# Kernel tuning notes

Measured on AMD Instinct MI355X. Metric: run time of the kernel, lower is better.

Reference implementation:

```python
import jax, jax.numpy as jnp
import numpy as np

THETA = 1.0       # spiking threshold (params['neuron']['theta'])
TAU_SR = 10.0     # SRM synaptic time constant (tauSr)
K = 100           # srm kernel support; alpha kernel has decayed to ~0 by 10*tau


def srm_kernel():
    # SLAYER SRMALPHA kernel: eps(t) = (t/tau) * exp(1 - t/tau), t = 0..K-1 (Ts = 1)
    t = jnp.arange(K, dtype=jnp.float32)
    return (t / TAU_SR) * jnp.exp(1.0 - t / TAU_SR)


def psp(x):
    # Causal temporal convolution with shared SRM kernel: y[t] = sum_s eps[s] * x[t-s]
    # x: [B, C, T]
    B, C, T = x.shape
    k = srm_kernel()[::-1].reshape(1, 1, K)  # flip: lax conv is correlation
    xr = x.reshape(B * C, 1, T)
    y = jax.lax.conv_general_dilated(xr, k, window_strides=(1,), padding=[(K - 1, 0)])
    return y.reshape(B, C, T)


def spike(u):
    # Hard threshold (forward of SLAYER spike function)
    return (u >= THETA).astype(u.dtype)


def setup_inputs() -> dict:
    key = jax.random.key(0)
    k1, k2, k3 = jax.random.split(key, 3)
    B, T = 256, 1000
    IN, HID, OUT = 78, 16, 20
    spike_input = (jax.random.uniform(k1, (B, IN, T)) < 0.1).astype(jnp.float32)
    W1 = jax.random.normal(k2, (HID, IN), dtype=jnp.float32) * 0.3
    W2 = jax.random.normal(k3, (OUT, HID), dtype=jnp.float32) * 0.3
    return {"spike_input": spike_input, "W1": W1, "W2": W2}


def reference(spike_input, W1, W2):
    # layer 1: dense (per-timestep matmul) -> psp temporal filter -> spike threshold
    u1 = psp(jnp.einsum('hi,bit->bht', W1, spike_input))  # [B, HID, T]
    s1 = spike(u1)
    # layer 2
    u2 = psp(jnp.einsum('oh,bht->bot', W2, s1))           # [B, OUT, T]
    return spike(u2)
```

## Files before the change

### kernel.cpp

```cpp
#include <hip/hip_runtime.h>
#include <math.h>


#define B_     256
#define IN_    78
#define HID_   16
#define OUT_   20
#define T_     1000
#define TT_    125
#define J_     224
#define ZSTR_  228
#define XSTR_  260

#define GRP(EP, A0,A1,A2,A3, B0,B1,B2,B3, C0,C1,C2) { \
  const double2 e01_ = *(const double2*)(EP); \
  const double2 e23_ = *(const double2*)((EP)+2); \
  u0 += e01_.x*(A3); u1 += e01_.x*(B0); u2 += e01_.x*(B1); u3 += e01_.x*(B2); \
  u4 += e01_.x*(B3); u5 += e01_.x*(C0); u6 += e01_.x*(C1); u7 += e01_.x*(C2); \
  u0 += e01_.y*(A2); u1 += e01_.y*(A3); u2 += e01_.y*(B0); u3 += e01_.y*(B1); \
  u4 += e01_.y*(B2); u5 += e01_.y*(B3); u6 += e01_.y*(C0); u7 += e01_.y*(C1); \
  u0 += e23_.x*(A1); u1 += e23_.x*(A2); u2 += e23_.x*(A3); u3 += e23_.x*(B0); \
  u4 += e23_.x*(B1); u5 += e23_.x*(B2); u6 += e23_.x*(B3); u7 += e23_.x*(C0); \
  u0 += e23_.y*(A0); u1 += e23_.y*(A1); u2 += e23_.y*(A2); u3 += e23_.y*(A3); \
  u4 += e23_.y*(B0); u5 += e23_.y*(B1); u6 += e23_.y*(B2); u7 += e23_.y*(B3); }

#define LOADF(X0,X1,X2,X3, P) { \
  const float4 lf_ = *(const float4*)(P); \
  X0 = (double)lf_.x; X1 = (double)lf_.y; X2 = (double)lf_.z; X3 = (double)lf_.w; }

__device__ __forceinline__ void init_eps_d(double* eps_d, int tid) {
  if (tid < 100) {
    float a = (float)tid / 10.0f;
    float e = a * expf(1.0f - a);
    eps_d[tid] = (double)e;
  }
}

#define MMROW(XR, W0, W1) { \
  const float2 f0_ = *(const float2*)((XR)); \
  const float2 f1_ = *(const float2*)((XR) + 64); \
  const float2 f2_ = *(const float2*)((XR) + 128); \
  const float2 f3_ = *(const float2*)((XR) + 192); \
  const double x0_=(double)f0_.x, x1_=(double)f0_.y; \
  const double x2_=(double)f1_.x, x3_=(double)f1_.y; \
  const double x4_=(double)f2_.x, x5_=(double)f2_.y; \
  const double x6_=(double)f3_.x, x7_=(double)f3_.y; \
  m00 += (W0)*x0_; m01 += (W0)*x1_; m02 += (W0)*x2_; m03 += (W0)*x3_; \
  m04 += (W0)*x4_; m05 += (W0)*x5_; m06 += (W0)*x6_; m07 += (W0)*x7_; \
  m10 += (W1)*x0_; m11 += (W1)*x1_; m12 += (W1)*x2_; m13 += (W1)*x3_; \
  m14 += (W1)*x4_; m15 += (W1)*x5_; m16 += (W1)*x6_; m17 += (W1)*x7_; }

#define STORE2(BASE, EOFF, MA, MB) \
  if (tb + (EOFF) < T_ - 1) \
    *(float2*)&zout[(BASE) + (size_t)(tb + (EOFF))] = \
        make_float2((float)(MA), (float)(MB));

__global__ __launch_bounds__(256) void mm1(
    const float* __restrict__ x, const float* __restrict__ W1,
    float* __restrict__ zout)
{
  __shared__ float  xs[13 * XSTR_];
  __shared__ double wd[16 * 80];

  const int tid = threadIdx.x;
  const int b   = blockIdx.x >> 2;
  const int tc  = blockIdx.x & 3;
  const int tcb = tc * 256;

  for (int idx = tid; idx < HID_ * IN_; idx += 256)
    wd[(idx / IN_) * 80 + (idx % IN_)] = (double)W1[idx];

  const int  t_c = tcb + tid;
  const bool cok = (t_c < T_);
  const int p = tid >> 5;
  const int q = tid & 31;

  double m00=0,m01=0,m02=0,m03=0,m04=0,m05=0,m06=0,m07=0;
  double m10=0,m11=0,m12=0,m13=0,m14=0,m15=0,m16=0,m17=0;

  for (int ci = 0; ci < 6; ++ci) {
    __syncthreads();
    {
      const float* xp = x + ((size_t)b * IN_ + ci * 13) * T_ + t_c;
#pragma unroll
      for (int r = 0; r < 13; ++r)
        xs[r * XSTR_ + tid] = cok ? xp[r * T_] : 0.0f;
    }
    __syncthreads();
    const int wbase0 = (2*p)     * 80 + ci * 13;
    const int wbase1 = (2*p + 1) * 80 + ci * 13;
#pragma unroll
    for (int i = 0; i < 13; ++i) {
      const float* xr = &xs[i * XSTR_ + 2 * q];
      const double w0 = wd[wbase0 + i];
      const double w1 = wd[wbase1 + i];
      MMROW(xr, w0, w1)
    }
  }

  const size_t r0 = ((size_t)b * HID_ + 2*p) * T_;
  const size_t r1 = r0 + T_;
  const int tb = tcb + 2 * q;
  STORE2(r0,   0, m00, m01)  STORE2(r0,  64, m02, m03)
  STORE2(r0, 128, m04, m05)  STORE2(r0, 192, m06, m07)
  STORE2(r1,   0, m10, m11)  STORE2(r1,  64, m12, m13)
  STORE2(r1, 128, m14, m15)  STORE2(r1, 192, m16, m17)
}

__global__ __launch_bounds__(256) void mm2(
    const float* __restrict__ s1, const float* __restrict__ W2,
    float* __restrict__ zout)
{
  __shared__ float  ss[16 * XSTR_];
  __shared__ double wd[OUT_ * HID_];

  const int tid = threadIdx.x;
  const int b   = blockIdx.x >> 2;
  const int tc  = blockIdx.x & 3;
  const int tcb = tc * 256;

  for (int idx = tid; idx < OUT_ * HID_; idx += 256)
    wd[idx] = (double)W2[idx];

  const int  t_c = tcb + tid;
  const bool cok = (t_c < T_);
  {
    const float* sp = s1 + (size_t)b * HID_ * T_ + t_c;
#pragma unroll
    for (int r = 0; r < HID_; ++r)
      ss[r * XSTR_ + tid] = cok ? sp[r * T_] : 0.0f;
  }
  __syncthreads();

  const int p = tid >> 5;
  const int q = tid & 31;
  const int tb = tcb + 2 * q;

  for (int pg = p; pg < 10; pg += 8) {
    double m00=0,m01=0,m02=0,m03=0,m04=0,m05=0,m06=0,m07=0;
    double m10=0,m11=0,m12=0,m13=0,m14=0,m15=0,m16=0,m17=0;
    const int wbase0 = (2*pg)     * HID_;
    const int wbase1 = (2*pg + 1) * HID_;
#pragma unroll
    for (int i = 0; i < HID_; ++i) {
      const float* xr = &ss[i * XSTR_ + 2 * q];
      const double w0 = wd[wbase0 + i];
      const double w1 = wd[wbase1 + i];
      MMROW(xr, w0, w1)
    }
    const size_t r0 = ((size_t)b * OUT_ + 2*pg) * T_;
    const size_t r1 = r0 + T_;
    STORE2(r0,   0, m00, m01)  STORE2(r0,  64, m02, m03)
    STORE2(r0, 128, m04, m05)  STORE2(r0, 192, m06, m07)
    STORE2(r1,   0, m10, m11)  STORE2(r1,  64, m12, m13)
    STORE2(r1, 128, m14, m15)  STORE2(r1, 192, m16, m17)
  }
}

__global__ __launch_bounds__(256) void fir_g(
    const float* __restrict__ zin, float* __restrict__ sout,
    int R, int tile_fixed)
{
  __shared__ float zf[OUT_ * ZSTR_];
  __shared__ __align__(16) double eps_d[100];

  const int tid  = threadIdx.x;
  const int b    = (tile_fixed >= 0) ? (int)blockIdx.x : (int)(blockIdx.x >> 3);
  const int tile = (tile_fixed >= 0) ? tile_fixed      : (int)(blockIdx.x & 7);
  const int t0   = tile * TT_;

  init_eps_d(eps_d, tid);
  for (int idx = tid; idx < R * ZSTR_; idx += 256) {
    const int cc = idx % ZSTR_;
    const int t  = t0 - 99 + cc;
    const int r  = idx / ZSTR_;
    zf[idx] = (cc < J_ && t >= 0) ? zin[((size_t)b * R + r) * T_ + t] : 0.0f;
  }
  __syncthreads();

  for (int task = tid; task < R * 16; task += 256) {
    const int h = task >> 4, q = task & 15;
    const float* zrow = &zf[h * ZSTR_ + 8 * q];
    double u0=0,u1=0,u2=0,u3=0,u4=0,u5=0,u6=0,u7=0;
    double A0,A1,A2,A3,B0,B1,B2,B3,C0,C1,C2,C3;
    LOADF(A0,A1,A2,A3, zrow + 96);
    LOADF(B0,B1,B2,B3, zrow + 100);
    LOADF(C0,C1,C2,C3, zrow + 104);
    GRP(eps_d, A0,A1,A2,A3, B0,B1,B2,B3, C0,C1,C2)

    const float*  zp = zrow + 92;
    const double* ep = eps_d + 4;
#pragma unroll 1
    for (int k = 0; k < 8; ++k) {
      LOADF(C0,C1,C2,C3, zp);
      GRP(ep,     C0,C1,C2,C3, A0,A1,A2,A3, B0,B1,B2)
      LOADF(B0,B1,B2,B3, zp - 4);
      GRP(ep + 4, B0,B1,B2,B3, C0,C1,C2,C3, A0,A1,A2)
      LOADF(A0,A1,A2,A3, zp - 8);
      GRP(ep + 8, A0,A1,A2,A3, B0,B1,B2,B3, C0,C1,C2)
      zp -= 12; ep += 12;
    }

    const size_t base = ((size_t)b * R + h) * T_ + t0 + 8 * q;
    const int tb = 8 * q;
    const float f0=(float)u0, f1=(float)u1, f2=(float)u2, f3=(float)u3;
    const float f4=(float)u4, f5=(float)u5, f6=(float)u6, f7=(float)u7;
    sout[base + 0] = (f0 >= 1.0f) ? 1.0f : 0.0f;
    sout[base + 1] = (f1 >= 1.0f) ? 1.0f : 0.0f;
    sout[base + 2] = (f2 >= 1.0f) ? 1.0f : 0.0f;
    sout[base + 3] = (f3 >= 1.0f) ? 1.0f : 0.0f;
    if (tb + 4 < TT_) sout[base + 4] = (f4 >= 1.0f) ? 1.0f : 0.0f;
    if (tb + 5 < TT_) sout[base + 5] = (f5 >= 1.0f) ? 1.0f : 0.0f;
    if (tb + 6 < TT_) sout[base + 6] = (f6 >= 1.0f) ? 1.0f : 0.0f;
    if (tb + 7 < TT_) sout[base + 7] = (f7 >= 1.0f) ? 1.0f : 0.0f;
  }
}

extern "C" void kernel_launch(void* const* d_in, const int* in_sizes, int n_in,
                              void* d_out, int out_size, void* d_ws, size_t ws_size,
                              hipStream_t stream) {
  const float* x  = (const float*)d_in[0];
  const float* W1 = (const float*)d_in[1];
  const float* W2 = (const float*)d_in[2];
  float* outp = (float*)d_out;
  float* base = (float*)d_ws;

  const size_t Z1E = (size_t)B_ * HID_ * T_;
  const size_t Z2E = (size_t)B_ * OUT_ * T_;

  if (ws_size >= (Z1E + Z2E) * sizeof(float)) {
    float* z1 = base;
    float* s1 = base + Z2E;
    float* z2 = base;
    mm1<<<dim3(B_ * 4), dim3(256), 0, stream>>>(x, W1, z1);
    fir_g<<<dim3(B_ * 8), dim3(256), 0, stream>>>(z1, s1, HID_, -1);
    mm2<<<dim3(B_ * 4), dim3(256), 0, stream>>>(s1, W2, z2);
    fir_g<<<dim3(B_ * 8), dim3(256), 0, stream>>>(z2, outp, OUT_, -1);
  } else if (ws_size >= 2 * Z1E * sizeof(float)) {
    float* z1 = base;
    float* s1 = base + Z1E;
    mm1<<<dim3(B_ * 4), dim3(256), 0, stream>>>(x, W1, z1);
    fir_g<<<dim3(B_ * 8), dim3(256), 0, stream>>>(z1, s1, HID_, -1);
    mm2<<<dim3(B_ * 4), dim3(256), 0, stream>>>(s1, W2, outp);
    for (int k = 7; k >= 0; --k)
      fir_g<<<dim3(B_), dim3(256), 0, stream>>>(outp, outp, OUT_, k);
  } else {
    float* z1 = base;
    mm1<<<dim3(B_ * 4), dim3(256), 0, stream>>>(x, W1, z1);
    for (int k = 7; k >= 0; --k)
      fir_g<<<dim3(B_), dim3(256), 0, stream>>>(z1, z1, HID_, k);
    mm2<<<dim3(B_ * 4), dim3(256), 0, stream>>>(z1, W2, outp);
    for (int k = 7; k >= 0; --k)
      fir_g<<<dim3(B_), dim3(256), 0, stream>>>(outp, outp, OUT_, k);
  }
}
```

Before: 122.6 us.

## Halve time tile in mm kernels and prefetch next input chunk into registers

The two channel-mixing kernels now cover 128 timesteps per block instead of 256, which doubles the grid and halves the per-thread accumulators from 16 to 8 doubles. The load pattern changes so that 256 threads cover 128 columns by two rows each. mm1 also software-pipelines its six input-channel chunks: the next chunk's global loads go into registers before the current chunk's FMAs run. The aim is more parallelism and latency hiding, at the cost of more blocks and more redundant weight staging into shared memory per block.

```diff
diff --git a/kernel.cpp b/kernel.cpp
--- a/kernel.cpp
+++ b/kernel.cpp
@@ -10,7 +10,8 @@
 #define TT_    125
 #define J_     224
 #define ZSTR_  228
-#define XSTR_  260
+#define TC_    128
+#define MSTR_  132
 
 #define GRP(EP, A0,A1,A2,A3, B0,B1,B2,B3, C0,C1,C2) { \
   const double2 e01_ = *(const double2*)(EP); \
@@ -36,19 +37,13 @@
   }
 }
 
-#define MMROW(XR, W0, W1) { \
-  const float2 f0_ = *(const float2*)((XR)); \
+#define MMROW2(XR, W0, W1) { \
+  const float2 f0_ = *(const float2*)(XR); \
   const float2 f1_ = *(const float2*)((XR) + 64); \
-  const float2 f2_ = *(const float2*)((XR) + 128); \
-  const float2 f3_ = *(const float2*)((XR) + 192); \
   const double x0_=(double)f0_.x, x1_=(double)f0_.y; \
   const double x2_=(double)f1_.x, x3_=(double)f1_.y; \
-  const double x4_=(double)f2_.x, x5_=(double)f2_.y; \
-  const double x6_=(double)f3_.x, x7_=(double)f3_.y; \
   m00 += (W0)*x0_; m01 += (W0)*x1_; m02 += (W0)*x2_; m03 += (W0)*x3_; \
-  m04 += (W0)*x4_; m05 += (W0)*x5_; m06 += (W0)*x6_; m07 += (W0)*x7_; \
-  m10 += (W1)*x0_; m11 += (W1)*x1_; m12 += (W1)*x2_; m13 += (W1)*x3_; \
-  m14 += (W1)*x4_; m15 += (W1)*x5_; m16 += (W1)*x6_; m17 += (W1)*x7_; }
+  m10 += (W1)*x0_; m11 += (W1)*x1_; m12 += (W1)*x2_; m13 += (W1)*x3_; }
 
 #define STORE2(BASE, EOFF, MA, MB) \
   if (tb + (EOFF) < T_ - 1) \
@@ -59,101 +54,112 @@
     const float* __restrict__ x, const float* __restrict__ W1,
     float* __restrict__ zout)
 {
-  __shared__ float  xs[13 * XSTR_];
+  __shared__ float  xs[13 * MSTR_];
   __shared__ double wd[16 * 80];
 
   const int tid = threadIdx.x;
-  const int b   = blockIdx.x >> 2;
-  const int tc  = blockIdx.x & 3;
-  const int tcb = tc * 256;
+  const int b   = blockIdx.x >> 3;
+  const int tc  = blockIdx.x & 7;
+  const int tcb = tc * TC_;
 
   for (int idx = tid; idx < HID_ * IN_; idx += 256)
     wd[(idx / IN_) * 80 + (idx % IN_)] = (double)W1[idx];
 
-  const int  t_c = tcb + tid;
-  const bool cok = (t_c < T_);
+  const int  c_  = tid & 127;
+  const int  r0_ = tid >> 7;
+  const int  tg_ = tcb + c_;
+  const bool tok = (tg_ < T_);
+  const bool t6  = tok && (r0_ == 0);
+
   const int p = tid >> 5;
   const int q = tid & 31;
 
-  double m00=0,m01=0,m02=0,m03=0,m04=0,m05=0,m06=0,m07=0;
-  double m10=0,m11=0,m12=0,m13=0,m14=0,m15=0,m16=0,m17=0;
-
+  double m00=0,m01=0,m02=0,m03=0,m10=0,m11=0,m12=0,m13=0;
+  float g0,g1,g2,g3,g4,g5,g6;
+
+#define ISSUE_MM1(CI) { \
+    const float* xb_ = x + ((size_t)b * IN_ + (CI) * 13 + r0_) * T_ + tg_; \
+    g0 = tok ? xb_[0]       : 0.0f; \
+    g1 = tok ? xb_[2  * T_] : 0.0f; \
+    g2 = tok ? xb_[4  * T_] : 0.0f; \
+    g3 = tok ? xb_[6  * T_] : 0.0f; \
+    g4 = tok ? xb_[8  * T_] : 0.0f; \
+    g5 = tok ? xb_[10 * T_] : 0.0f; \
+    g6 = t6  ? xb_[12 * T_] : 0.0f; }
+
+  ISSUE_MM1(0)
   for (int ci = 0; ci < 6; ++ci) {
     __syncthreads();
     {
-      const float* xp = x + ((size_t)b * IN_ + ci * 13) * T_ + t_c;
-#pragma unroll
-      for (int r = 0; r < 13; ++r)
-        xs[r * XSTR_ + tid] = cok ? xp[r * T_] : 0.0f;
+      float* dst = &xs[r0_ * MSTR_ + c_];
+      dst[0]          = g0;  dst[2  * MSTR_] = g1;
+      dst[4  * MSTR_] = g2;  dst[6  * MSTR_] = g3;
+      dst[8  * MSTR_] = g4;  dst[10 * MSTR_] = g5;
+      if (r0_ == 0) dst[12 * MSTR_] = g6;
     }
     __syncthreads();
+    if (ci < 5) ISSUE_MM1(ci + 1)
     const int wbase0 = (2*p)     * 80 + ci * 13;
     const int wbase1 = (2*p + 1) * 80 + ci * 13;
 #pragma unroll
     for (int i = 0; i < 13; ++i) {
-      const float* xr = &xs[i * XSTR_ + 2 * q];
-      const double w0 = wd[wbase0 + i];
-      const double w1 = wd[wbase1 + i];
-      MMROW(xr, w0, w1)
-    }
-  }
-
-  const size_t r0 = ((size_t)b * HID_ + 2*p) * T_;
-  const size_t r1 = r0 + T_;
+      const float* xr = &xs[i * MSTR_ + 2 * q];
+      MMROW2(xr, wd[wbase0 + i], wd[wbase1 + i])
+    }
+  }
+
+  const size_t r0s = ((size_t)b * HID_ + 2*p) * T_;
+  const size_t r1s = r0s + T_;
   const int tb = tcb + 2 * q;
-  STORE2(r0,   0, m00, m01)  STORE2(r0,  64, m02, m03)
-  STORE2(r0, 128, m04, m05)  STORE2(r0, 192, m06, m07)
-  STORE2(r1,   0, m10, m11)  STORE2(r1,  64, m12, m13)
-  STORE2(r1, 128, m14, m15)  STORE2(r1, 192, m16, m17)
+  STORE2(r0s,  0, m00, m01)  STORE2(r0s, 64, m02, m03)
+  STORE2(r1s,  0, m10, m11)  STORE2(r1s, 64, m12, m13)
 }
 
 __global__ __launch_bounds__(256) void mm2(
     const float* __restrict__ s1, const float* __restrict__ W2,
     float* __restrict__ zout)
 {
-  __shared__ float  ss[16 * XSTR_];
+  __shared__ float  ss[16 * MSTR_];
   __shared__ double wd[OUT_ * HID_];
 
   const int tid = threadIdx.x;
-  const int b   = blockIdx.x >> 2;
-  const int tc  = blockIdx.x & 3;
-  const int tcb = tc * 256;
+  const int b   = blockIdx.x >> 3;
+  const int tc  = blockIdx.x & 7;
+  const int tcb = tc * TC_;
 
   for (int idx = tid; idx < OUT_ * HID_; idx += 256)
     wd[idx] = (double)W2[idx];
 
-  const int  t_c = tcb + tid;
-  const bool cok = (t_c < T_);
   {
-    const float* sp = s1 + (size_t)b * HID_ * T_ + t_c;
+    const int  c_  = tid & 127;
+    const int  r0_ = tid >> 7;
+    const int  tg_ = tcb + c_;
+    const bool tok = (tg_ < T_);
+    const float* sb = s1 + ((size_t)b * HID_ + r0_) * T_ + tg_;
+    float* dst = &ss[r0_ * MSTR_ + c_];
 #pragma unroll
-    for (int r = 0; r < HID_; ++r)
-      ss[r * XSTR_ + tid] = cok ? sp[r * T_] : 0.0f;
+    for (int e = 0; e < 8; ++e)
+      dst[2 * e * MSTR_] = tok ? sb[2 * e * T_] : 0.0f;
   }
   __syncthreads();
 
-  const int p = tid >> 5;
-  const int q = tid & 31;
+  const int p  = tid >> 5;
+  const int q  = tid & 31;
   const int tb = tcb + 2 * q;
 
   for (int pg = p; pg < 10; pg += 8) {
-    double m00=0,m01=0,m02=0,m03=0,m04=0,m05=0,m06=0,m07=0;
-    double m10=0,m11=0,m12=0,m13=0,m14=0,m15=0,m16=0,m17=0;
+    double m00=0,m01=0,m02=0,m03=0,m10=0,m11=0,m12=0,m13=0;
     const int wbase0 = (2*pg)     * HID_;
     const int wbase1 = (2*pg + 1) * HID_;
 #pragma unroll
     for (int i = 0; i < HID_; ++i) {
-      const float* xr = &ss[i * XSTR_ + 2 * q];
-      const double w0 = wd[wbase0 + i];
-      const double w1 = wd[wbase1 + i];
-      MMROW(xr, w0, w1)
-    }
-    const size_t r0 = ((size_t)b * OUT_ + 2*pg) * T_;
-    const size_t r1 = r0 + T_;
-    STORE2(r0,   0, m00, m01)  STORE2(r0,  64, m02, m03)
-    STORE2(r0, 128, m04, m05)  STORE2(r0, 192, m06, m07)
-    STORE2(r1,   0, m10, m11)  STORE2(r1,  64, m12, m13)
-    STORE2(r1, 128, m14, m15)  STORE2(r1, 192, m16, m17)
+      const float* xr = &ss[i * MSTR_ + 2 * q];
+      MMROW2(xr, wd[wbase0 + i], wd[wbase1 + i])
+    }
+    const size_t r0s = ((size_t)b * OUT_ + 2*pg) * T_;
+    const size_t r1s = r0s + T_;
+    STORE2(r0s,  0, m00, m01)  STORE2(r0s, 64, m02, m03)
+    STORE2(r1s,  0, m10, m11)  STORE2(r1s, 64, m12, m13)
   }
 }
 
@@ -232,24 +238,24 @@
     float* z1 = base;
     float* s1 = base + Z2E;
     float* z2 = base;
-    mm1<<<dim3(B_ * 4), dim3(256), 0, stream>>>(x, W1, z1);
+    mm1<<<dim3(B_ * 8), dim3(256), 0, stream>>>(x, W1, z1);
     fir_g<<<dim3(B_ * 8), dim3(256), 0, stream>>>(z1, s1, HID_, -1);
-    mm2<<<dim3(B_ * 4), dim3(256), 0, stream>>>(s1, W2, z2);
+    mm2<<<dim3(B_ * 8), dim3(256), 0, stream>>>(s1, W2, z2);
     fir_g<<<dim3(B_ * 8), dim3(256), 0, stream>>>(z2, outp, OUT_, -1);
   } else if (ws_size >= 2 * Z1E * sizeof(float)) {
     float* z1 = base;
     float* s1 = base + Z1E;
-    mm1<<<dim3(B_ * 4), dim3(256), 0, stream>>>(x, W1, z1);
+    mm1<<<dim3(B_ * 8), dim3(256), 0, stream>>>(x, W1, z1);
     fir_g<<<dim3(B_ * 8), dim3(256), 0, stream>>>(z1, s1, HID_, -1);
-    mm2<<<dim3(B_ * 4), dim3(256), 0, stream>>>(s1, W2, outp);
+    mm2<<<dim3(B_ * 8), dim3(256), 0, stream>>>(s1, W2, outp);
     for (int k = 7; k >= 0; --k)
       fir_g<<<dim3(B_), dim3(256), 0, stream>>>(outp, outp, OUT_, k);
   } else {
     float* z1 = base;
-    mm1<<<dim3(B_ * 4), dim3(256), 0, stream>>>(x, W1, z1);
+    mm1<<<dim3(B_ * 8), dim3(256), 0, stream>>>(x, W1, z1);
     for (int k = 7; k >= 0; --k)
       fir_g<<<dim3(B_), dim3(256), 0, stream>>>(z1, z1, HID_, k);
-    mm2<<<dim3(B_ * 4), dim3(256), 0, stream>>>(z1, W2, outp);
+    mm2<<<dim3(B_ * 8), dim3(256), 0, stream>>>(z1, W2, outp);
     for (int k = 7; k >= 0; --k)
       fir_g<<<dim3(B_), dim3(256), 0, stream>>>(outp, outp, OUT_, k);
   }
```

After: 109.8 us. 1.12x faster.

## Fuse per-layer matmul with temporal FIR and spike into single kernels

Applied to the files above, without the earlier changes.

Merges each layer's dense matmul with its PSP convolution and threshold into one kernel per layer, tiled by batch and 125-step time windows with a 99-step halo. The pre-activation z stays in shared memory instead of making a round trip through global memory, and the launch count drops from four to two. In exchange, each tile recomputes the matmul over its halo region (224 columns computed for 125 outputs), and the larger shared-memory footprint per block may lower occupancy.

```diff
diff --git a/kernel.cpp b/kernel.cpp
--- a/kernel.cpp
+++ b/kernel.cpp
@@ -27,6 +27,25 @@
 #define LOADF(X0,X1,X2,X3, P) { \
   const float4 lf_ = *(const float4*)(P); \
   X0 = (double)lf_.x; X1 = (double)lf_.y; X2 = (double)lf_.z; X3 = (double)lf_.w; }
+
+#define FIR_BODY(ZROW) { \
+  double A0,A1,A2,A3,B0,B1,B2,B3,C0,C1,C2,C3; \
+  LOADF(A0,A1,A2,A3, (ZROW) + 96); \
+  LOADF(B0,B1,B2,B3, (ZROW) + 100); \
+  LOADF(C0,C1,C2,C3, (ZROW) + 104); \
+  GRP(eps_d, A0,A1,A2,A3, B0,B1,B2,B3, C0,C1,C2) \
+  const float*  zp_ = (ZROW) + 92; \
+  const double* ep_ = eps_d + 4; \
+  _Pragma("unroll 1") \
+  for (int k_ = 0; k_ < 8; ++k_) { \
+    LOADF(C0,C1,C2,C3, zp_); \
+    GRP(ep_,     C0,C1,C2,C3, A0,A1,A2,A3, B0,B1,B2) \
+    LOADF(B0,B1,B2,B3, zp_ - 4); \
+    GRP(ep_ + 4, B0,B1,B2,B3, C0,C1,C2,C3, A0,A1,A2) \
+    LOADF(A0,A1,A2,A3, zp_ - 8); \
+    GRP(ep_ + 8, A0,A1,A2,A3, B0,B1,B2,B3, C0,C1,C2) \
+    zp_ -= 12; ep_ += 12; \
+  } }
 
 __device__ __forceinline__ void init_eps_d(double* eps_d, int tid) {
   if (tid < 100) {
@@ -50,28 +69,40 @@
   m10 += (W1)*x0_; m11 += (W1)*x1_; m12 += (W1)*x2_; m13 += (W1)*x3_; \
   m14 += (W1)*x4_; m15 += (W1)*x5_; m16 += (W1)*x6_; m17 += (W1)*x7_; }
 
-#define STORE2(BASE, EOFF, MA, MB) \
-  if (tb + (EOFF) < T_ - 1) \
-    *(float2*)&zout[(BASE) + (size_t)(tb + (EOFF))] = \
-        make_float2((float)(MA), (float)(MB));
-
-__global__ __launch_bounds__(256) void mm1(
+#define ZSTORE_PAIR(ZBASE0) { \
+  float* z0_ = (ZBASE0); \
+  float* z1_ = z0_ + ZSTR_; \
+  *(float2*)(z0_)       = make_float2((float)m00, (float)m01); \
+  *(float2*)(z0_ + 64)  = make_float2((float)m02, (float)m03); \
+  *(float2*)(z0_ + 128) = make_float2((float)m04, (float)m05); \
+  *(float2*)(z1_)       = make_float2((float)m10, (float)m11); \
+  *(float2*)(z1_ + 64)  = make_float2((float)m12, (float)m13); \
+  *(float2*)(z1_ + 128) = make_float2((float)m14, (float)m15); \
+  if (q < 16) { \
+    *(float2*)(z0_ + 192) = make_float2((float)m06, (float)m07); \
+    *(float2*)(z1_ + 192) = make_float2((float)m16, (float)m17); \
+  } }
+
+__global__ __launch_bounds__(256) void l1f(
     const float* __restrict__ x, const float* __restrict__ W1,
-    float* __restrict__ zout)
+    float* __restrict__ sout)
 {
   __shared__ float  xs[13 * XSTR_];
+  __shared__ float  zf[HID_ * ZSTR_];
   __shared__ double wd[16 * 80];
-
-  const int tid = threadIdx.x;
-  const int b   = blockIdx.x >> 2;
-  const int tc  = blockIdx.x & 3;
-  const int tcb = tc * 256;
-
+  __shared__ __align__(16) double eps_d[100];
+
+  const int tid  = threadIdx.x;
+  const int b    = blockIdx.x >> 3;
+  const int tile = blockIdx.x & 7;
+  const int t0   = tile * TT_;
+
+  init_eps_d(eps_d, tid);
   for (int idx = tid; idx < HID_ * IN_; idx += 256)
     wd[(idx / IN_) * 80 + (idx % IN_)] = (double)W1[idx];
-
-  const int  t_c = tcb + tid;
-  const bool cok = (t_c < T_);
+  if (tid < HID_ * 4)
+    zf[(tid >> 2) * ZSTR_ + 224 + (tid & 3)] = 0.0f;
+
   const int p = tid >> 5;
   const int q = tid & 31;
 
@@ -80,129 +111,31 @@
 
   for (int ci = 0; ci < 6; ++ci) {
     __syncthreads();
-    {
-      const float* xp = x + ((size_t)b * IN_ + ci * 13) * T_ + t_c;
-#pragma unroll
-      for (int r = 0; r < 13; ++r)
-        xs[r * XSTR_ + tid] = cok ? xp[r * T_] : 0.0f;
+    for (int idx = tid; idx < 13 * XSTR_; idx += 256) {
+      const int r = idx / XSTR_, cc = idx % XSTR_;
+      const int t = t0 - 99 + cc;
+      xs[idx] = (cc < J_ && t >= 0)
+                  ? x[((size_t)b * IN_ + ci * 13 + r) * T_ + t] : 0.0f;
     }
     __syncthreads();
-    const int wbase0 = (2*p)     * 80 + ci * 13;
-    const int wbase1 = (2*p + 1) * 80 + ci * 13;
+    const int wb0 = (2*p) * 80 + ci * 13;
+    const int wb1 = wb0 + 80;
 #pragma unroll
     for (int i = 0; i < 13; ++i) {
       const float* xr = &xs[i * XSTR_ + 2 * q];
-      const double w0 = wd[wbase0 + i];
-      const double w1 = wd[wbase1 + i];
-      MMROW(xr, w0, w1)
+      MMROW(xr, wd[wb0 + i], wd[wb1 + i])
     }
   }
-
-  const size_t r0 = ((size_t)b * HID_ + 2*p) * T_;
-  const size_t r1 = r0 + T_;
-  const int tb = tcb + 2 * q;
-  STORE2(r0,   0, m00, m01)  STORE2(r0,  64, m02, m03)
-  STORE2(r0, 128, m04, m05)  STORE2(r0, 192, m06, m07)
-  STORE2(r1,   0, m10, m11)  STORE2(r1,  64, m12, m13)
-  STORE2(r1, 128, m14, m15)  STORE2(r1, 192, m16, m17)
-}
-
-__global__ __launch_bounds__(256) void mm2(
-    const float* __restrict__ s1, const float* __restrict__ W2,
-    float* __restrict__ zout)
-{
-  __shared__ float  ss[16 * XSTR_];
-  __shared__ double wd[OUT_ * HID_];
-
-  const int tid = threadIdx.x;
-  const int b   = blockIdx.x >> 2;
-  const int tc  = blockIdx.x & 3;
-  const int tcb = tc * 256;
-
-  for (int idx = tid; idx < OUT_ * HID_; idx += 256)
-    wd[idx] = (double)W2[idx];
-
-  const int  t_c = tcb + tid;
-  const bool cok = (t_c < T_);
+  ZSTORE_PAIR(&zf[(2*p) * ZSTR_ + 2 * q])
+  __syncthreads();
+
   {
-    const float* sp = s1 + (size_t)b * HID_ * T_ + t_c;
-#pragma unroll
-    for (int r = 0; r < HID_; ++r)
-      ss[r * XSTR_ + tid] = cok ? sp[r * T_] : 0.0f;
-  }
-  __syncthreads();
-
-  const int p = tid >> 5;
-  const int q = tid & 31;
-  const int tb = tcb + 2 * q;
-
-  for (int pg = p; pg < 10; pg += 8) {
-    double m00=0,m01=0,m02=0,m03=0,m04=0,m05=0,m06=0,m07=0;
-    double m10=0,m11=0,m12=0,m13=0,m14=0,m15=0,m16=0,m17=0;
-    const int wbase0 = (2*pg)     * HID_;
-    const int wbase1 = (2*pg + 1) * HID_;
-#pragma unroll
-    for (int i = 0; i < HID_; ++i) {
-      const float* xr = &ss[i * XSTR_ + 2 * q];
-      const double w0 = wd[wbase0 + i];
-      const double w1 = wd[wbase1 + i];
-      MMROW(xr, w0, w1)
-    }
-    const size_t r0 = ((size_t)b * OUT_ + 2*pg) * T_;
-    const size_t r1 = r0 + T_;
-    STORE2(r0,   0, m00, m01)  STORE2(r0,  64, m02, m03)
-    STORE2(r0, 128, m04, m05)  STORE2(r0, 192, m06, m07)
-    STORE2(r1,   0, m10, m11)  STORE2(r1,  64, m12, m13)
-    STORE2(r1, 128, m14, m15)  STORE2(r1, 192, m16, m17)
-  }
-}
-
-__global__ __launch_bounds__(256) void fir_g(
-    const float* __restrict__ zin, float* __restrict__ sout,
-    int R, int tile_fixed)
-{
-  __shared__ float zf[OUT_ * ZSTR_];
-  __shared__ __align__(16) double eps_d[100];
-
-  const int tid  = threadIdx.x;
-  const int b    = (tile_fixed >= 0) ? (int)blockIdx.x : (int)(blockIdx.x >> 3);
-  const int tile = (tile_fixed >= 0) ? tile_fixed      : (int)(blockIdx.x & 7);
-  const int t0   = tile * TT_;
-
-  init_eps_d(eps_d, tid);
-  for (int idx = tid; idx < R * ZSTR_; idx += 256) {
-    const int cc = idx % ZSTR_;
-    const int t  = t0 - 99 + cc;
-    const int r  = idx / ZSTR_;
-    zf[idx] = (cc < J_ && t >= 0) ? zin[((size_t)b * R + r) * T_ + t] : 0.0f;
-  }
-  __syncthreads();
-
-  for (int task = tid; task < R * 16; task += 256) {
-    const int h = task >> 4, q = task & 15;
-    const float* zrow = &zf[h * ZSTR_ + 8 * q];
+    const int h = tid >> 4, q16 = tid & 15;
+    const float* zrow = &zf[h * ZSTR_ + 8 * q16];
     double u0=0,u1=0,u2=0,u3=0,u4=0,u5=0,u6=0,u7=0;
-    double A0,A1,A2,A3,B0,B1,B2,B3,C0,C1,C2,C3;
-    LOADF(A0,A1,A2,A3, zrow + 96);
-    LOADF(B0,B1,B2,B3, zrow + 100);
-    LOADF(C0,C1,C2,C3, zrow + 104);
-    GRP(eps_d, A0,A1,A2,A3, B0,B1,B2,B3, C0,C1,C2)
-
-    const float*  zp = zrow + 92;
-    const double* ep = eps_d + 4;
-#pragma unroll 1
-    for (int k = 0; k < 8; ++k) {
-      LOADF(C0,C1,C2,C3, zp);
-      GRP(ep,     C0,C1,C2,C3, A0,A1,A2,A3, B0,B1,B2)
-      LOADF(B0,B1,B2,B3, zp - 4);
-      GRP(ep + 4, B0,B1,B2,B3, C0,C1,C2,C3, A0,A1,A2)
-      LOADF(A0,A1,A2,A3, zp - 8);
-      GRP(ep + 8, A0,A1,A2,A3, B0,B1,B2,B3, C0,C1,C2)
-      zp -= 12; ep += 12;
-    }
-
-    const size_t base = ((size_t)b * R + h) * T_ + t0 + 8 * q;
-    const int tb = 8 * q;
+    FIR_BODY(zrow)
+    const size_t base = ((size_t)b * HID_ + h) * T_ + t0 + 8 * q16;
+    const int tb = 8 * q16;
     const float f0=(float)u0, f1=(float)u1, f2=(float)u2, f3=(float)u3;
     const float f4=(float)u4, f5=(float)u5, f6=(float)u6, f7=(float)u7;
     sout[base + 0] = (f0 >= 1.0f) ? 1.0f : 0.0f;
@@ -216,6 +149,70 @@
   }
 }
 
+__global__ __launch_bounds__(256) void l2f(
+    const float* __restrict__ s1, const float* __restrict__ W2,
+    float* __restrict__ outp)
+{
+  __shared__ float  ss[HID_ * XSTR_];
+  __shared__ float  zf[OUT_ * ZSTR_];
+  __shared__ double wd[OUT_ * HID_];
+  __shared__ __align__(16) double eps_d[100];
+
+  const int tid  = threadIdx.x;
+  const int b    = blockIdx.x >> 3;
+  const int tile = blockIdx.x & 7;
+  const int t0   = tile * TT_;
+
+  init_eps_d(eps_d, tid);
+  for (int idx = tid; idx < OUT_ * HID_; idx += 256)
+    wd[idx] = (double)W2[idx];
+  if (tid < OUT_ * 4)
+    zf[(tid >> 2) * ZSTR_ + 224 + (tid & 3)] = 0.0f;
+  for (int idx = tid; idx < HID_ * XSTR_; idx += 256) {
+    const int r = idx / XSTR_, cc = idx % XSTR_;
+    const int t = t0 - 99 + cc;
+    ss[idx] = (cc < J_ && t >= 0)
+                ? s1[((size_t)b * HID_ + r) * T_ + t] : 0.0f;
+  }
+  __syncthreads();
+
+  const int p = tid >> 5;
+  const int q = tid & 31;
+
+  for (int pg = p; pg < 10; pg += 8) {
+    double m00=0,m01=0,m02=0,m03=0,m04=0,m05=0,m06=0,m07=0;
+    double m10=0,m11=0,m12=0,m13=0,m14=0,m15=0,m16=0,m17=0;
+    const int wb0 = (2*pg) * HID_;
+    const int wb1 = wb0 + HID_;
+#pragma unroll
+    for (int i = 0; i < HID_; ++i) {
+      const float* xr = &ss[i * XSTR_ + 2 * q];
+      MMROW(xr, wd[wb0 + i], wd[wb1 + i])
+    }
+    ZSTORE_PAIR(&zf[(2*pg) * ZSTR_ + 2 * q])
+  }
+  __syncthreads();
+
+  for (int task = tid; task < OUT_ * 16; task += 256) {
+    const int h = task >> 4, q16 = task & 15;
+    const float* zrow = &zf[h * ZSTR_ + 8 * q16];
+    double u0=0,u1=0,u2=0,u3=0,u4=0,u5=0,u6=0,u7=0;
+    FIR_BODY(zrow)
+    const size_t base = ((size_t)b * OUT_ + h) * T_ + t0 + 8 * q16;
+    const int tb = 8 * q16;
+    const float f0=(float)u0, f1=(float)u1, f2=(float)u2, f3=(float)u3;
+    const float f4=(float)u4, f5=(float)u5, f6=(float)u6, f7=(float)u7;
+    outp[base + 0] = (f0 >= 1.0f) ? 1.0f : 0.0f;
+    outp[base + 1] = (f1 >= 1.0f) ? 1.0f : 0.0f;
+    outp[base + 2] = (f2 >= 1.0f) ? 1.0f : 0.0f;
+    outp[base + 3] = (f3 >= 1.0f) ? 1.0f : 0.0f;
+    if (tb + 4 < TT_) outp[base + 4] = (f4 >= 1.0f) ? 1.0f : 0.0f;
+    if (tb + 5 < TT_) outp[base + 5] = (f5 >= 1.0f) ? 1.0f : 0.0f;
+    if (tb + 6 < TT_) outp[base + 6] = (f6 >= 1.0f) ? 1.0f : 0.0f;
+    if (tb + 7 < TT_) outp[base + 7] = (f7 >= 1.0f) ? 1.0f : 0.0f;
+  }
+}
+
 extern "C" void kernel_launch(void* const* d_in, const int* in_sizes, int n_in,
                               void* d_out, int out_size, void* d_ws, size_t ws_size,
                               hipStream_t stream) {
@@ -223,34 +220,8 @@
   const float* W1 = (const float*)d_in[1];
   const float* W2 = (const float*)d_in[2];
   float* outp = (float*)d_out;
-  float* base = (float*)d_ws;
-
-  const size_t Z1E = (size_t)B_ * HID_ * T_;
-  const size_t Z2E = (size_t)B_ * OUT_ * T_;
-
-  if (ws_size >= (Z1E + Z2E) * sizeof(float)) {
-    float* z1 = base;
-    float* s1 = base + Z2E;
-    float* z2 = base;
-    mm1<<<dim3(B_ * 4), dim3(256), 0, stream>>>(x, W1, z1);
-    fir_g<<<dim3(B_ * 8), dim3(256), 0, stream>>>(z1, s1, HID_, -1);
-    mm2<<<dim3(B_ * 4), dim3(256), 0, stream>>>(s1, W2, z2);
-    fir_g<<<dim3(B_ * 8), dim3(256), 0, stream>>>(z2, outp, OUT_, -1);
-  } else if (ws_size >= 2 * Z1E * sizeof(float)) {
-    float* z1 = base;
-    float* s1 = base + Z1E;
-    mm1<<<dim3(B_ * 4), dim3(256), 0, stream>>>(x, W1, z1);
-    fir_g<<<dim3(B_ * 8), dim3(256), 0, stream>>>(z1, s1, HID_, -1);
-    mm2<<<dim3(B_ * 4), dim3(256), 0, stream>>>(s1, W2, outp);
-    for (int k = 7; k >= 0; --k)
-      fir_g<<<dim3(B_), dim3(256), 0, stream>>>(outp, outp, OUT_, k);
-  } else {
-    float* z1 = base;
-    mm1<<<dim3(B_ * 4), dim3(256), 0, stream>>>(x, W1, z1);
-    for (int k = 7; k >= 0; --k)
-      fir_g<<<dim3(B_), dim3(256), 0, stream>>>(z1, z1, HID_, k);
-    mm2<<<dim3(B_ * 4), dim3(256), 0, stream>>>(z1, W2, outp);
-    for (int k = 7; k >= 0; --k)
-      fir_g<<<dim3(B_), dim3(256), 0, stream>>>(outp, outp, OUT_, k);
-  }
-}
+  float* s1   = (float*)d_ws;
+
+  l1f<<<dim3(B_ * 8), dim3(256), 0, stream>>>(x,  W1, s1);
+  l2f<<<dim3(B_ * 8), dim3(256), 0, stream>>>(s1, W2, outp);
+}
```

After: 265.5 us. +116.6%, slower.
